# Optimization experiments

Hardware: AMD Instinct MI355X
Metric: run time of the kernel (lower is better)

The kernel has to match this reference:

```python
import jax, jax.numpy as jnp
import numpy as np

HEADS = 16
ROPE_BASE = 10000.0


def _rope(x):
    # x: [b, h, n, d]. lucidrains partial rotary: RotaryEmbedding(head_dim//2)
    # rotates only the first rot_dim = d//2 channels, interleaved-pair style.
    d = x.shape[-1]
    rot = d // 2
    inv_freq = 1.0 / (ROPE_BASE ** (jnp.arange(0, rot, 2, dtype=jnp.float32) / rot))  # [rot//2]
    pos = jnp.arange(x.shape[2], dtype=jnp.float32)
    freqs = pos[:, None] * inv_freq[None, :]                  # [n, rot//2]
    cos, sin = jnp.cos(freqs), jnp.sin(freqs)
    xr, xp = x[..., :rot], x[..., rot:]
    x1, x2 = xr[..., 0::2], xr[..., 1::2]                     # interleaved pairs
    o1 = x1 * cos - x2 * sin
    o2 = x2 * cos + x1 * sin
    xr_out = jnp.stack([o1, o2], axis=-1).reshape(xr.shape)   # re-interleave
    return jnp.concatenate([xr_out, xp], axis=-1)


def setup_inputs() -> dict:
    key = jax.random.key(0)
    k0, k1 = jax.random.split(key)
    B, N, D = 2, 2048, 2048
    x = jax.random.normal(k0, (B, N, D), dtype=jnp.float32)
    W_qkv = jax.random.normal(k1, (3 * D, D), dtype=jnp.float32) * (D ** -0.5)
    b_qkv = jnp.zeros((3 * D,), dtype=jnp.float32)
    return {"x": x, "W_qkv": W_qkv, "b_qkv": b_qkv}


def reference(x, W_qkv, b_qkv):
    B, N, D = x.shape
    H = HEADS
    hd = D // H
    qkv = x @ W_qkv.T + b_qkv                                  # [b, n, 3d]
    q, k, v = jnp.split(qkv, 3, axis=-1)
    to_heads = lambda t: t.reshape(B, N, H, hd).transpose(0, 2, 1, 3)  # b h n d
    q, k, v = to_heads(q), to_heads(k), to_heads(v)
    q, k = _rope(q), _rope(k)
    scale = 1.0 / np.sqrt(hd)
    scores = jnp.einsum('bhnd,bhmd->bhnm', q, k) * scale
    causal = jnp.tril(jnp.ones((N, N), dtype=bool))
    scores = jnp.where(causal, scores, -jnp.inf)
    attn = jax.nn.softmax(scores, axis=-1)
    y = jnp.einsum('bhnm,bhmd->bhnd', attn, v)
    return y.transpose(0, 2, 1, 3).reshape(B, N, D)
```

## Files before the change

kernel.cpp:

```cpp
#include <hip/hip_runtime.h>
#include <hip/hip_bf16.h>
#include <math.h>

typedef unsigned short u16;
typedef unsigned int u32;
typedef __attribute__((ext_vector_type(8))) short bf16x8;
typedef __attribute__((ext_vector_type(4))) float f32x4;

#define B_ 2
#define N_ 2048
#define D_ 2048
#define H_ 16
#define HD 128
#define GK 2048

__device__ __forceinline__ u16 f2bf(float f) {
  u32 u = __float_as_uint(f);
  u = (u + 0x7fffu + ((u >> 16) & 1u)) >> 16;
  return (u16)u;
}

__device__ __forceinline__ u32 cvtpk(float lo, float hi) {
  u32 r;
  asm("v_cvt_pk_bf16_f32 %0, %1, %2" : "=v"(r) : "v"(lo), "v"(hi));
  return r;
}

__device__ __forceinline__ void gload_lds16(const void* g, void* l) {
  __builtin_amdgcn_global_load_lds(
      (const __attribute__((address_space(1))) u32*)g,
      (__attribute__((address_space(3))) u32*)l, 16, 0, 0);
}

__global__ __launch_bounds__(256) void cvt_kernel(const float* __restrict__ in,
                                                  u16* __restrict__ out, int n4) {
  int i = blockIdx.x * blockDim.x + threadIdx.x;
  int st = gridDim.x * blockDim.x;
  for (; i < n4; i += st) {
    float4 v = ((const float4*)in)[i];
    ushort4 o;
    o.x = f2bf(v.x); o.y = f2bf(v.y); o.z = f2bf(v.z); o.w = f2bf(v.w);
    ((ushort4*)out)[i] = o;
  }
}

__global__ __launch_bounds__(256) void rope_tbl_kernel(float* __restrict__ tbl) {
  int i = blockIdx.x * blockDim.x + threadIdx.x;
  if (i >= N_ * 32) return;
  int pos = i >> 5, p = i & 31;
  double inv = pow(10000.0, -(double)p / 32.0);
  double a = (double)pos * inv;
  tbl[2 * i]     = (float)cos(a);
  tbl[2 * i + 1] = (float)sin(a);
}

__global__ __launch_bounds__(512, 2) void qkv_gemm_kernel(
    const u16* __restrict__ X, const u16* __restrict__ W,
    const float* __restrict__ bias, const float* __restrict__ tbl,
    u16* __restrict__ Qo, u16* __restrict__ Ko, u16* __restrict__ Vo) {
  __shared__ char smem[147456];
  const int tid = threadIdx.x;
  const int lane = tid & 63;
  const int w = tid >> 6;
  const int wm = w >> 2, wn = w & 3;
  const int l15 = lane & 15, l4 = lane >> 4;

  const int bid = blockIdx.x;
  const int wg = (bid & 7) * 64 + (bid >> 3);
  const int n0 = (wg & 31) * 192;
  const int m0 = (wg >> 5) * 256;

  const int aof0 = (l4 * 16) ^ ((l15 & 7) << 4);
  const int aof1 = (64 + l4 * 16) ^ ((l15 & 7) << 4);

  int srowA[2], scolA[2];
#pragma unroll
  for (int p = 0; p < 2; ++p) {
    int o = (w * 2 + p) * 1024 + lane * 16;
    int lo = o ^ (((o >> 7) & 7) << 4);
    srowA[p] = lo >> 7;
    scolA[p] = (lo & 127) >> 1;
  }
  const int oB = w * 1024 + lane * 16;
  const int loB = oB ^ (((oB >> 7) & 7) << 4);
  const int srowB = loB >> 7, scolB = (loB & 127) >> 1;

  f32x4 acc[8][3];
#pragma unroll
  for (int fm = 0; fm < 8; ++fm)
#pragma unroll
    for (int fn = 0; fn < 3; ++fn)
#pragma unroll
      for (int q = 0; q < 4; ++q) acc[fm][fn][q] = 0.f;

  auto stageA = [&](char* Abase, int half, int k0) {
#pragma unroll
    for (int p = 0; p < 2; ++p) {
      gload_lds16(X + (size_t)(m0 + half * 128 + srowA[p]) * GK + k0 + scolA[p],
                  Abase + half * 16384 + (w * 2 + p) * 1024);
    }
  };
  auto stageB = [&](char* Bbase, int chunk, int k0) {
    gload_lds16(W + (size_t)(n0 + chunk * 64 + srowB) * GK + k0 + scolB,
                Bbase + chunk * 8192 + w * 1024);
  };

  const int NK = GK / 64;

  stageA(smem, 0, 0); stageA(smem, 1, 0);
  stageB(smem + 98304, 0, 0); stageB(smem + 98304, 1, 0); stageB(smem + 98304, 2, 0);
  stageA(smem + 32768, 0, 64); stageA(smem + 32768, 1, 64);
  asm volatile("s_waitcnt vmcnt(4)" ::: "memory");
  __builtin_amdgcn_s_barrier();

  int at = 0;
  for (int T = 0; T < NK; ++T) {
    const int bt = T & 1;
    int an2 = at + 2; if (an2 >= 3) an2 -= 3;
    const char* Ab = smem + at * 32768 + wm * 16384;
    const char* Bb = smem + 98304 + bt * 24576;
    char* Bn = smem + 98304 + (bt ^ 1) * 24576;
    char* An = smem + an2 * 32768;
    const int kn1 = (T + 1) * 64, kn2 = (T + 2) * 64;
    const bool hasB = (T + 1 < NK), hasA = (T + 2 < NK);

    bf16x8 b[3], a[4];

#pragma unroll
    for (int fn = 0; fn < 3; ++fn)
      b[fn] = *(const bf16x8*)(Bb + (wn * 48 + fn * 16 + l15) * 128 + aof0);
#pragma unroll
    for (int fm = 0; fm < 4; ++fm)
      a[fm] = *(const bf16x8*)(Ab + (fm * 16 + l15) * 128 + aof0);
    if (hasB) { stageB(Bn, 0, kn1); stageB(Bn, 1, kn1); }
    __builtin_amdgcn_s_barrier();
    __builtin_amdgcn_s_setprio(1);
#pragma unroll
    for (int fm = 0; fm < 4; ++fm)
#pragma unroll
      for (int fn = 0; fn < 3; ++fn)
        acc[fm][fn] = __builtin_amdgcn_mfma_f32_16x16x32_bf16(a[fm], b[fn], acc[fm][fn], 0, 0, 0);
    __builtin_amdgcn_s_setprio(0);
    __builtin_amdgcn_s_barrier();

#pragma unroll
    for (int fm = 0; fm < 4; ++fm)
      a[fm] = *(const bf16x8*)(Ab + ((fm + 4) * 16 + l15) * 128 + aof0);
    if (hasB) stageB(Bn, 2, kn1);
    __builtin_amdgcn_s_barrier();
    __builtin_amdgcn_s_setprio(1);
#pragma unroll
    for (int fm = 0; fm < 4; ++fm)
#pragma unroll
      for (int fn = 0; fn < 3; ++fn)
        acc[fm + 4][fn] = __builtin_amdgcn_mfma_f32_16x16x32_bf16(a[fm], b[fn], acc[fm + 4][fn], 0, 0, 0);
    __builtin_amdgcn_s_setprio(0);
    __builtin_amdgcn_s_barrier();

#pragma unroll
    for (int fn = 0; fn < 3; ++fn)
      b[fn] = *(const bf16x8*)(Bb + (wn * 48 + fn * 16 + l15) * 128 + aof1);
#pragma unroll
    for (int fm = 0; fm < 4; ++fm)
      a[fm] = *(const bf16x8*)(Ab + (fm * 16 + l15) * 128 + aof1);
    if (hasA) stageA(An, 0, kn2);
    __builtin_amdgcn_s_barrier();
    __builtin_amdgcn_s_setprio(1);
#pragma unroll
    for (int fm = 0; fm < 4; ++fm)
#pragma unroll
      for (int fn = 0; fn < 3; ++fn)
        acc[fm][fn] = __builtin_amdgcn_mfma_f32_16x16x32_bf16(a[fm], b[fn], acc[fm][fn], 0, 0, 0);
    __builtin_amdgcn_s_setprio(0);
    __builtin_amdgcn_s_barrier();

#pragma unroll
    for (int fm = 0; fm < 4; ++fm)
      a[fm] = *(const bf16x8*)(Ab + ((fm + 4) * 16 + l15) * 128 + aof1);
    if (hasA) {
      stageA(An, 1, kn2);
      asm volatile("s_waitcnt vmcnt(4)" ::: "memory");
    } else {
      asm volatile("s_waitcnt vmcnt(0)" ::: "memory");
    }
    __builtin_amdgcn_s_barrier();
    __builtin_amdgcn_s_setprio(1);
#pragma unroll
    for (int fm = 0; fm < 4; ++fm)
#pragma unroll
      for (int fn = 0; fn < 3; ++fn)
        acc[fm + 4][fn] = __builtin_amdgcn_mfma_f32_16x16x32_bf16(a[fm], b[fn], acc[fm + 4][fn], 0, 0, 0);
    __builtin_amdgcn_s_setprio(0);
    __builtin_amdgcn_s_barrier();

    at = (at + 1 == 3) ? 0 : at + 1;
  }

  const float QSCALE = 0.08838834764831845f;
#pragma unroll
  for (int fn = 0; fn < 3; ++fn) {
    int gn = n0 + wn * 48 + fn * 16 + l15;
    float bv = bias[gn];
    int sec = gn >> 11;
    int wi = gn & 2047;
    int h = wi >> 7;
    int d = wi & 127;
    u16* dstbase = (sec == 0) ? Qo : (sec == 1) ? Ko : Vo;
    float mulf = (sec == 0) ? QSCALE : 1.f;
    bool doRope = (sec < 2) && (d < 64);
    int pidx = d >> 1;
    bool odd = (d & 1) != 0;
#pragma unroll
    for (int fm = 0; fm < 8; ++fm) {
#pragma unroll
      for (int j = 0; j < 4; ++j) {
        int gm = m0 + wm * 128 + fm * 16 + l4 * 4 + j;
        int bb = gm >> 11;
        int pos = gm & 2047;
        float v = acc[fm][fn][j] + bv;
        float pr = __shfl_xor(v, 1);
        float ov = v;
        if (doRope) {
          float2 cs = ((const float2*)tbl)[pos * 32 + pidx];
          ov = odd ? (v * cs.x + pr * cs.y) : (v * cs.x - pr * cs.y);
        }
        dstbase[(size_t)((bb * H_ + h) * N_ + pos) * HD + d] = f2bf(ov * mulf);
      }
    }
  }
}

__global__ __launch_bounds__(256, 2) void flash_kernel(
    const u16* __restrict__ Q, const u16* __restrict__ K, const u16* __restrict__ V,
    float* __restrict__ Out) {
  __shared__ char smem[69632];

  const int tid = threadIdx.x, lane = tid & 63, w = tid >> 6;
  const int l15 = lane & 15, l4 = lane >> 4;

  const int bid = blockIdx.x;
  const int xcd = bid & 7, slot = bid >> 3;
  const int bh = xcd * 4 + (slot >> 4);
  const int x = 15 - (slot & 15);
  const int bb = bh >> 4, h = bh & 15;
  const size_t base = (size_t)bh * (N_ * HD);
  const int q0 = x * 128;
  const int nt = 2 * x + 2;

  bf16x8 qf[2][4];
#pragma unroll
  for (int g = 0; g < 2; ++g) {
    const u16* qp = Q + base + (size_t)(q0 + w * 32 + g * 16 + l15) * HD + l4 * 8;
#pragma unroll
    for (int kf = 0; kf < 4; ++kf) qf[g][kf] = *(const bf16x8*)(qp + kf * 32);
  }

  float m_r[2] = {-1e30f, -1e30f}, l_r[2] = {0.f, 0.f};
  f32x4 accO[2][8];
#pragma unroll
  for (int g = 0; g < 2; ++g)
#pragma unroll
    for (int df = 0; df < 8; ++df)
#pragma unroll
      for (int q = 0; q < 4; ++q) accO[g][df][q] = 0.f;

  auto stageK = [&](int buf, int t0) {
    const u16* kb = K + base + (size_t)t0 * HD;
    char* kt = smem + buf * 16384;
#pragma unroll
    for (int i = 0; i < 4; ++i) {
      int c = w * 4 + i;
      int o = c * 1024 + lane * 16;
      int lo = o ^ (((o >> 8) & 7) << 4);
      gload_lds16(kb + (lo >> 1), kt + c * 1024);
    }
  };
  auto loadV = [&](int t0, bf16x8* vr) {
    const u16* vp = V + base + (size_t)(t0 + lane) * HD + w * 32;
#pragma unroll
    for (int i = 0; i < 4; ++i) vr[i] = *(const bf16x8*)(vp + i * 8);
  };
  auto writeV = [&](int buf, const bf16x8* vr) {
    u16* vt = (u16*)(smem + 32768 + buf * 18432);
#pragma unroll
    for (int i = 0; i < 4; ++i)
#pragma unroll
      for (int jj = 0; jj < 8; ++jj)
        vt[(w * 32 + i * 8 + jj) * 72 + lane] = (u16)vr[i][jj];
  };

  const int src0 = l15 + 32 * (l4 & 1);
  const int src1 = src0 + 16;
  const int half = l4 >> 1;
  union U8 { u32 u[4]; bf16x8 v; };

  bf16x8 vreg[4];
  stageK(0, 0);
  loadV(0, vreg);
  writeV(0, vreg);
  __syncthreads();

  for (int t = 0; t < nt; ++t) {
    const int cur = t & 1;
    const int t0 = t * 64;
    const bool pre = (t + 1 < nt);
    if (pre) { stageK(cur ^ 1, t0 + 64); loadV(t0 + 64, vreg); }

    const char* kt = smem + cur * 16384;
    const u16* vt = (const u16*)(smem + 32768 + cur * 18432);

    f32x4 s[2][4];
#pragma unroll
    for (int cf = 0; cf < 4; ++cf) {
#pragma unroll
      for (int q = 0; q < 4; ++q) { s[0][cf][q] = 0.f; s[1][cf][q] = 0.f; }
      int row = cf * 16 + l15;
      int sw = (row & 7) << 4;
#pragma unroll
      for (int kf = 0; kf < 4; ++kf) {
        int off = (row * 256 + kf * 64 + l4 * 16) ^ sw;
        bf16x8 kfrag = *(const bf16x8*)(kt + off);
        s[0][cf] = __builtin_amdgcn_mfma_f32_16x16x32_bf16(kfrag, qf[0][kf], s[0][cf], 0, 0, 0);
        s[1][cf] = __builtin_amdgcn_mfma_f32_16x16x32_bf16(kfrag, qf[1][kf], s[1][cf], 0, 0, 0);
      }
    }

    u32 pk[2][4][2];
#pragma unroll
    for (int g = 0; g < 2; ++g) {
      const int qbase = q0 + w * 32 + g * 16;
      if (t0 + 63 > qbase) {
        const int qg = qbase + l15;
#pragma unroll
        for (int cf = 0; cf < 4; ++cf)
#pragma unroll
          for (int j = 0; j < 4; ++j) {
            int kvg = t0 + cf * 16 + l4 * 4 + j;
            if (kvg > qg) s[g][cf][j] = -1e30f;
          }
      }
      float pmax = s[g][0][0];
#pragma unroll
      for (int cf = 0; cf < 4; ++cf)
#pragma unroll
        for (int j = 0; j < 4; ++j) pmax = fmaxf(pmax, s[g][cf][j]);
      pmax = fmaxf(pmax, __shfl_xor(pmax, 16));
      pmax = fmaxf(pmax, __shfl_xor(pmax, 32));

      if (!__all(pmax <= m_r[g] + 8.f)) {
        float mn = fmaxf(m_r[g], pmax);
        float rs = __expf(m_r[g] - mn);
        m_r[g] = mn;
        l_r[g] *= rs;
#pragma unroll
        for (int df = 0; df < 8; ++df)
#pragma unroll
          for (int j = 0; j < 4; ++j) accO[g][df][j] *= rs;
      }

      float ps = 0.f;
#pragma unroll
      for (int cf = 0; cf < 4; ++cf) {
        float p0 = __expf(s[g][cf][0] - m_r[g]);
        float p1 = __expf(s[g][cf][1] - m_r[g]);
        float p2 = __expf(s[g][cf][2] - m_r[g]);
        float p3 = __expf(s[g][cf][3] - m_r[g]);
        ps += (p0 + p1) + (p2 + p3);
        pk[g][cf][0] = cvtpk(p0, p1);
        pk[g][cf][1] = cvtpk(p2, p3);
      }
      ps += __shfl_xor(ps, 16);
      ps += __shfl_xor(ps, 32);
      l_r[g] += ps;
    }

#pragma unroll
    for (int c = 0; c < 2; ++c) {
      const int c2 = 2 * c;
      U8 pu[2];
#pragma unroll
      for (int g = 0; g < 2; ++g) {
        u32 a0 = (u32)__shfl((int)pk[g][c2][0], src0);
        u32 b0 = (u32)__shfl((int)pk[g][c2 + 1][0], src0);
        u32 a1 = (u32)__shfl((int)pk[g][c2][1], src0);
        u32 b1 = (u32)__shfl((int)pk[g][c2 + 1][1], src0);
        u32 a2 = (u32)__shfl((int)pk[g][c2][0], src1);
        u32 b2 = (u32)__shfl((int)pk[g][c2 + 1][0], src1);
        u32 a3 = (u32)__shfl((int)pk[g][c2][1], src1);
        u32 b3 = (u32)__shfl((int)pk[g][c2 + 1][1], src1);
        pu[g].u[0] = half ? b0 : a0;
        pu[g].u[1] = half ? b1 : a1;
        pu[g].u[2] = half ? b2 : a2;
        pu[g].u[3] = half ? b3 : a3;
      }
#pragma unroll
      for (int df = 0; df < 8; ++df) {
        bf16x8 vf = *(const bf16x8*)(vt + (df * 16 + l15) * 72 + c * 32 + l4 * 8);
        accO[0][df] = __builtin_amdgcn_mfma_f32_16x16x32_bf16(vf, pu[0].v, accO[0][df], 0, 0, 0);
        accO[1][df] = __builtin_amdgcn_mfma_f32_16x16x32_bf16(vf, pu[1].v, accO[1][df], 0, 0, 0);
      }
    }

    if (pre) writeV(cur ^ 1, vreg);
    __syncthreads();
  }

  float* Obuf = (float*)(smem + w * 8448);
  const int l31 = lane & 31;
#pragma unroll
  for (int g = 0; g < 2; ++g) {
    float inv = 1.f / l_r[g];
#pragma unroll
    for (int df = 0; df < 8; ++df) {
      f32x4 v = accO[g][df];
#pragma unroll
      for (int j = 0; j < 4; ++j) v[j] *= inv;
      *(f32x4*)&Obuf[l15 * 132 + df * 16 + l4 * 4] = v;
    }
#pragma unroll
    for (int p = 0; p < 8; ++p) {
      int row = p * 2 + (lane >> 5);
      f32x4 v = *(const f32x4*)&Obuf[row * 132 + l31 * 4];
      int qg = q0 + w * 32 + g * 16 + row;
      *(f32x4*)&Out[(size_t)(bb * N_ + qg) * D_ + h * HD + l31 * 4] = v;
    }
  }
}

extern "C" void kernel_launch(void* const* d_in, const int* in_sizes, int n_in,
                              void* d_out, int out_size, void* d_ws, size_t ws_size,
                              hipStream_t stream) {
  const float* x  = (const float*)d_in[0];
  const float* Wq = (const float*)d_in[1];
  const float* bq = (const float*)d_in[2];
  float* out = (float*)d_out;
  char* ws = (char*)d_ws;

  u16* Qb  = (u16*)(ws);
  u16* Kb  = (u16*)(ws + 16777216);
  u16* Vb  = (u16*)(ws + 2 * 16777216);
  u16* Xb  = (u16*)(ws + 3 * 16777216);
  u16* Wb  = (u16*)(ws + 4 * 16777216);
  float* tbl = (float*)(ws + 4 * 16777216 + 25165824);

  cvt_kernel<<<2048, 256, 0, stream>>>(x, Xb, (B_ * N_ * D_) / 4);
  cvt_kernel<<<2048, 256, 0, stream>>>(Wq, Wb, (3 * D_ * D_) / 4);
  rope_tbl_kernel<<<(N_ * 32 + 255) / 256, 256, 0, stream>>>(tbl);
  qkv_gemm_kernel<<<512, 512, 0, stream>>>(Xb, Wb, bq, tbl, Qb, Kb, Vb);
  flash_kernel<<<512, 256, 0, stream>>>(Qb, Kb, Vb, out);
}
```

Baseline: 254.5 us.

## Drop intra-iteration barriers in QKV GEMM main loop, keep one per k-step

Removes seven of the eight workgroup barriers per k-iteration of the QKV projection GEMM, leaving only the final one. The global-to-LDS staging calls are regrouped into two bursts, and separate B fragment registers are kept for each half of the k-step. The aim is to cut barrier stalls so waves drift and overlap MFMA with LDS reads. The triple-buffered A and double-buffered B layout must now carry all synchronization, which risks LDS races and adds register pressure.

```diff
diff --git a/kernel.cpp b/kernel.cpp
--- a/kernel.cpp
+++ b/kernel.cpp
@@ -124,72 +124,63 @@
     const int kn1 = (T + 1) * 64, kn2 = (T + 2) * 64;
     const bool hasB = (T + 1 < NK), hasA = (T + 2 < NK);
 
-    bf16x8 b[3], a[4];
+    bf16x8 bl[3], bh[3], aq[4];
 
 #pragma unroll
     for (int fn = 0; fn < 3; ++fn)
-      b[fn] = *(const bf16x8*)(Bb + (wn * 48 + fn * 16 + l15) * 128 + aof0);
-#pragma unroll
-    for (int fm = 0; fm < 4; ++fm)
-      a[fm] = *(const bf16x8*)(Ab + (fm * 16 + l15) * 128 + aof0);
-    if (hasB) { stageB(Bn, 0, kn1); stageB(Bn, 1, kn1); }
-    __builtin_amdgcn_s_barrier();
+      bl[fn] = *(const bf16x8*)(Bb + (wn * 48 + fn * 16 + l15) * 128 + aof0);
+#pragma unroll
+    for (int fm = 0; fm < 4; ++fm)
+      aq[fm] = *(const bf16x8*)(Ab + (fm * 16 + l15) * 128 + aof0);
+    if (hasB) { stageB(Bn, 0, kn1); stageB(Bn, 1, kn1); stageB(Bn, 2, kn1); }
     __builtin_amdgcn_s_setprio(1);
 #pragma unroll
     for (int fm = 0; fm < 4; ++fm)
 #pragma unroll
       for (int fn = 0; fn < 3; ++fn)
-        acc[fm][fn] = __builtin_amdgcn_mfma_f32_16x16x32_bf16(a[fm], b[fn], acc[fm][fn], 0, 0, 0);
+        acc[fm][fn] = __builtin_amdgcn_mfma_f32_16x16x32_bf16(aq[fm], bl[fn], acc[fm][fn], 0, 0, 0);
     __builtin_amdgcn_s_setprio(0);
-    __builtin_amdgcn_s_barrier();
-
-#pragma unroll
-    for (int fm = 0; fm < 4; ++fm)
-      a[fm] = *(const bf16x8*)(Ab + ((fm + 4) * 16 + l15) * 128 + aof0);
-    if (hasB) stageB(Bn, 2, kn1);
-    __builtin_amdgcn_s_barrier();
+
+#pragma unroll
+    for (int fm = 0; fm < 4; ++fm)
+      aq[fm] = *(const bf16x8*)(Ab + ((fm + 4) * 16 + l15) * 128 + aof0);
     __builtin_amdgcn_s_setprio(1);
 #pragma unroll
     for (int fm = 0; fm < 4; ++fm)
 #pragma unroll
       for (int fn = 0; fn < 3; ++fn)
-        acc[fm + 4][fn] = __builtin_amdgcn_mfma_f32_16x16x32_bf16(a[fm], b[fn], acc[fm + 4][fn], 0, 0, 0);
+        acc[fm + 4][fn] = __builtin_amdgcn_mfma_f32_16x16x32_bf16(aq[fm], bl[fn], acc[fm + 4][fn], 0, 0, 0);
     __builtin_amdgcn_s_setprio(0);
-    __builtin_amdgcn_s_barrier();
 
 #pragma unroll
     for (int fn = 0; fn < 3; ++fn)
-      b[fn] = *(const bf16x8*)(Bb + (wn * 48 + fn * 16 + l15) * 128 + aof1);
-#pragma unroll
-    for (int fm = 0; fm < 4; ++fm)
-      a[fm] = *(const bf16x8*)(Ab + (fm * 16 + l15) * 128 + aof1);
-    if (hasA) stageA(An, 0, kn2);
-    __builtin_amdgcn_s_barrier();
+      bh[fn] = *(const bf16x8*)(Bb + (wn * 48 + fn * 16 + l15) * 128 + aof1);
+#pragma unroll
+    for (int fm = 0; fm < 4; ++fm)
+      aq[fm] = *(const bf16x8*)(Ab + (fm * 16 + l15) * 128 + aof1);
+    if (hasA) { stageA(An, 0, kn2); stageA(An, 1, kn2); }
     __builtin_amdgcn_s_setprio(1);
 #pragma unroll
     for (int fm = 0; fm < 4; ++fm)
 #pragma unroll
       for (int fn = 0; fn < 3; ++fn)
-        acc[fm][fn] = __builtin_amdgcn_mfma_f32_16x16x32_bf16(a[fm], b[fn], acc[fm][fn], 0, 0, 0);
+        acc[fm][fn] = __builtin_amdgcn_mfma_f32_16x16x32_bf16(aq[fm], bh[fn], acc[fm][fn], 0, 0, 0);
     __builtin_amdgcn_s_setprio(0);
-    __builtin_amdgcn_s_barrier();
-
-#pragma unroll
-    for (int fm = 0; fm < 4; ++fm)
-      a[fm] = *(const bf16x8*)(Ab + ((fm + 4) * 16 + l15) * 128 + aof1);
+
+#pragma unroll
+    for (int fm = 0; fm < 4; ++fm)
+      aq[fm] = *(const bf16x8*)(Ab + ((fm + 4) * 16 + l15) * 128 + aof1);
     if (hasA) {
-      stageA(An, 1, kn2);
       asm volatile("s_waitcnt vmcnt(4)" ::: "memory");
     } else {
       asm volatile("s_waitcnt vmcnt(0)" ::: "memory");
     }
-    __builtin_amdgcn_s_barrier();
     __builtin_amdgcn_s_setprio(1);
 #pragma unroll
     for (int fm = 0; fm < 4; ++fm)
 #pragma unroll
       for (int fn = 0; fn < 3; ++fn)
-        acc[fm + 4][fn] = __builtin_amdgcn_mfma_f32_16x16x32_bf16(a[fm], b[fn], acc[fm + 4][fn], 0, 0, 0);
+        acc[fm + 4][fn] = __builtin_amdgcn_mfma_f32_16x16x32_bf16(aq[fm], bh[fn], acc[fm + 4][fn], 0, 0, 0);
     __builtin_amdgcn_s_setprio(0);
     __builtin_amdgcn_s_barrier();
 
```

After: 251.0 us. Within noise of the previous version (-1.4%).
